# Kernel optimization log

Hardware: AMD Instinct MI355X
Metric: run time of the kernel (lower is better)

## Reference

```python
import jax, jax.numpy as jnp
import numpy as np

STDP_LR = 0.005
V_TH = 1.0  # IFNode default threshold, hard reset to 0


def setup_inputs() -> dict:
    key = jax.random.key(0)
    k1, k2 = jax.random.split(key)
    T, B, D, H = 50, 256, 1024, 2048
    x_seq = jax.random.uniform(k1, (T, B, D), dtype=jnp.float32)
    # Linear(D, H, bias=False) default init: U(-1/sqrt(D), 1/sqrt(D)), weight shape [H, D]
    bound = 1.0 / np.sqrt(D)
    weight = jax.random.uniform(k2, (H, D), dtype=jnp.float32, minval=-bound, maxval=bound)
    return {"x_seq": x_seq, "weight": weight}


def _spike(v_minus_th):
    # forward: Heaviside (surrogate only matters for backward)
    return (v_minus_th >= 0).astype(v_minus_th.dtype)


def reference(x_seq, weight):
    T, B, D = x_seq.shape
    H = weight.shape[0]
    inv_b = jnp.float32(1.0 / B)

    def step(carry, x):
        w, v = carry  # w: [H, D], v: [B, H] membrane potential (persists across t)
        mem = x @ w.T                      # [B, H]
        v = v + mem                        # IF integrate
        s = _spike(v - V_TH)               # [B, H] spikes
        v = v * (1.0 - s)                  # hard reset to 0 where spiked
        # dw.mean(0).T == lr * (1/B) * x^T s, shape [H, D] after transpose -> 'bi,bh->hi'
        dw = STDP_LR * inv_b * jnp.einsum('bi,bh->hi', x, s)
        w = w + dw                         # in-place .data update in torch
        return (w, v), s

    v0 = jnp.zeros((B, H), dtype=x_seq.dtype)
    (_, _), s_all = jax.lax.scan(step, (weight, v0), x_seq)
    spike_trace = s_all.sum(axis=0)        # [B, H]
    return spike_trace
```

## Files before the change

### kernel.cpp

```cpp
#include <hip/hip_runtime.h>
#include <hip/hip_bf16.h>


#define T_STEPS 50
#define BATCH   256
#define DIM     1024
#define HID     2048
#define HT      16
#define LR_OVER_B (0.005f / 256.0f)

#define SMEM_BYTES (65536 + 32768 + 32768 + 4096)

typedef __attribute__((ext_vector_type(8))) short short8v;
typedef __attribute__((ext_vector_type(4))) float f32x4;
typedef __attribute__((ext_vector_type(4))) int   i32x4;

static __device__ __forceinline__ ushort f32_to_bf16u(float f) {
    __hip_bfloat16 h = __float2bfloat16(f);
    return __builtin_bit_cast(unsigned short, h);
}
static __device__ __forceinline__ float bf16u_to_f32(ushort u) {
    __hip_bfloat16 h = __builtin_bit_cast(__hip_bfloat16, u);
    return __bfloat162float(h);
}

#define MFMA_B16 __builtin_amdgcn_mfma_f32_16x16x32_bf16
#define MFMA_I8  __builtin_amdgcn_mfma_i32_16x16x64_i8

__global__ __launch_bounds__(256) void prep_fwd(
    const float* __restrict__ x, ushort* __restrict__ XF)
{
    __shared__ float xs[16 * 1024];
    const int t  = blockIdx.x >> 4;
    const int bt = blockIdx.x & 15;
    const float* xrow = x + ((size_t)t * BATCH + bt * 16) * DIM;
    for (int i = threadIdx.x; i < 16 * 1024 / 4; i += 256)
        ((float4*)xs)[i] = ((const float4*)xrow)[i];
    __syncthreads();

    ushort* outb = XF + ((size_t)t * 16 + bt) * (32 * 2 * 512);
    for (int item = threadIdx.x; item < 32 * 64; item += 256) {
        const int c = item >> 6;
        const int l = item & 63;
        const int row = l & 15;
        const int col = c * 32 + (l >> 4) * 8;
        short8v hv, lv;
#pragma unroll
        for (int j = 0; j < 8; ++j) {
            float v = xs[row * 1024 + col + j];
            ushort h = f32_to_bf16u(v);
            hv[j] = (short)h;
            lv[j] = (short)f32_to_bf16u(v - bf16u_to_f32(h));
        }
        *(short8v*)(outb + ((size_t)c * 2 + 0) * 512 + l * 8) = hv;
        *(short8v*)(outb + ((size_t)c * 2 + 1) * 512 + l * 8) = lv;
    }
}

__global__ __launch_bounds__(256) void prep_xq(
    const float* __restrict__ x, unsigned char* __restrict__ XQ)
{
    __shared__ ushort q14[256 * 16];
    const int t  = blockIdx.x >> 6;
    const int dt = blockIdx.x & 63;
    {
        const int b = threadIdx.x;
        const float* src = x + ((size_t)t * BATCH + b) * DIM + dt * 16;
#pragma unroll
        for (int k = 0; k < 16; ++k) {
            int u = (int)(src[k] * 16384.0f + 0.5f);
            q14[b * 16 + k] = (ushort)(u > 16383 ? 16383 : u);
        }
    }
    __syncthreads();

    unsigned char* outb = XQ + ((size_t)t * 64 + dt) * 8192;
    const int c = threadIdx.x >> 6;
    const int l = threadIdx.x & 63;
    unsigned char hi16[16], lo16[16];
#pragma unroll
    for (int jj = 0; jj < 16; ++jj) {
        const int b2 = c * 64 + (l >> 4) * 16 + jj;
        ushort v = q14[b2 * 16 + (l & 15)];
        hi16[jj] = (unsigned char)(v >> 7);
        lo16[jj] = (unsigned char)(v & 127);
    }
    *(i32x4*)(outb + c * 2048 + l * 16)        = *(i32x4*)hi16;
    *(i32x4*)(outb + c * 2048 + 1024 + l * 16) = *(i32x4*)lo16;
}

__global__ __launch_bounds__(1024, 1) void stdp_big(
    const ushort* __restrict__ XF, const unsigned char* __restrict__ XQ,
    const float* __restrict__ weight, float* __restrict__ out)
{
    extern __shared__ char smem[];
    float*  wfs = (float*)smem;
    ushort* whF = (ushort*)(smem + 65536);
    ushort* wlF = whF + 32 * 512;
    unsigned char* slQ = (unsigned char*)(smem + 65536 + 32768 + 32768);

    const int tid  = threadIdx.x;
    const int lane = tid & 63;
    const int w    = tid >> 6;
    const int h0   = blockIdx.x * HT;

    const int fr = lane & 15;
    const int rq = (lane >> 4) * 4;

    for (int i = tid; i < 32 * 64; i += 1024) {
        const int cc  = i >> 6;
        const int l   = i & 63;
        const int row = l & 15;
        const int col = cc * 32 + (l >> 4) * 8;
        const float* src = &weight[(size_t)(h0 + row) * DIM + col];
        short8v hv, lv;
#pragma unroll
        for (int j = 0; j < 8; ++j) {
            float v = src[j];
            ushort h = f32_to_bf16u(v);
            hv[j] = (short)h;
            lv[j] = (short)f32_to_bf16u(v - bf16u_to_f32(h));
        }
        *(short8v*)&whF[cc * 512 + l * 8] = hv;
        *(short8v*)&wlF[cc * 512 + l * 8] = lv;
    }
    for (int i = tid; i < 64 * 64; i += 1024) {
        const int dt = i >> 6;
        const int l  = i & 63;
        const int h  = l & 15;
        const int d  = dt * 16 + (l >> 4) * 4;
        *(float4*)&wfs[(size_t)i * 4] =
            *(const float4*)&weight[(size_t)(h0 + h) * DIM + d];
    }
    __syncthreads();

    const f32x4 z4 = {0.f, 0.f, 0.f, 0.f};
    const i32x4 zi = {0, 0, 0, 0};
    f32x4 vmem = z4;
    f32x4 trc  = z4;

    short8v GA[2][2], GB[2][2];
    i32x4 FH[4], FL[4];

#define LDP(F, base, p) do { _Pragma("unroll") \
    for (int c_ = 0; c_ < 2; ++c_) { \
        const int cc_ = (p) * 2 + c_; \
        F[c_][0] = *(const short8v*)((base) + ((size_t)cc_ * 2 + 0) * 512); \
        F[c_][1] = *(const short8v*)((base) + ((size_t)cc_ * 2 + 1) * 512); } } while (0)

#define MFP(F, p) do { _Pragma("unroll") \
    for (int c_ = 0; c_ < 2; ++c_) { \
        const int cc_ = (p) * 2 + c_; \
        short8v bh_ = *(const short8v*)&whF[cc_ * 512 + lane * 8]; \
        short8v bl_ = *(const short8v*)&wlF[cc_ * 512 + lane * 8]; \
        acc = MFMA_B16(F[c_][0], bh_, acc, 0, 0, 0); \
        acc = MFMA_B16(F[c_][0], bl_, acc, 0, 0, 0); \
        acc = MFMA_B16(F[c_][1], bh_, acc, 0, 0, 0); } } while (0)

    {
        const ushort* wb0 = XF + (size_t)w * (32 * 2 * 512) + lane * 8;
        LDP(GA, wb0, 0);
    }

    for (int t = 0; t < T_STEPS; ++t) {
        const ushort* wbase = XF + (size_t)t * (16 * 32 * 2 * 512)
                            + (size_t)w * (32 * 2 * 512) + lane * 8;

        f32x4 acc = z4;
#pragma unroll 1
        for (int it = 0; it < 7; ++it) {
            LDP(GB, wbase, 2 * it + 1);
            MFP(GA, 2 * it);
            LDP(GA, wbase, 2 * it + 2);
            MFP(GB, 2 * it + 1);
        }
        LDP(GB, wbase, 15);
        MFP(GA, 14);
        MFP(GB, 15);

        {
            unsigned sword = 0;
#pragma unroll
            for (int j = 0; j < 4; ++j) {
                float nv = vmem[j] + acc[j];
                bool fire = (nv >= 1.0f);
                vmem[j] = fire ? 0.0f : nv;
                trc[j] += fire ? 1.0f : 0.0f;
                sword |= (fire ? 1u : 0u) << (8 * j);
            }
            *(unsigned*)&slQ[(w >> 2) * 1024 + ((w & 3) * 16 + fr) * 16 + rq] = sword;
        }

        if (t >= T_STEPS - 1) break;

        const unsigned char* xqt = XQ + (size_t)t * (64 * 8192);
        {
            const unsigned char* tb = xqt + (size_t)(w * 4) * 8192 + lane * 16;
#pragma unroll
            for (int c = 0; c < 4; ++c) {
                FH[c] = *(const i32x4*)(tb + c * 2048);
                FL[c] = *(const i32x4*)(tb + c * 2048 + 1024);
            }
        }

        __syncthreads();

#pragma unroll
        for (int q = 0; q < 4; ++q) {
            const int dt = w * 4 + q;
            i32x4 aH = zi, aL = zi;
#pragma unroll
            for (int c = 0; c < 4; ++c) {
                i32x4 sf = *(const i32x4*)&slQ[c * 1024 + lane * 16];
                aH = MFMA_I8(FH[c], sf, aH, 0, 0, 0);
                aL = MFMA_I8(FL[c], sf, aL, 0, 0, 0);
            }
            if (q < 3) {
                const unsigned char* tb = xqt + (size_t)(dt + 1) * 8192 + lane * 16;
#pragma unroll
                for (int c = 0; c < 4; ++c) {
                    FH[c] = *(const i32x4*)(tb + c * 2048);
                    FL[c] = *(const i32x4*)(tb + c * 2048 + 1024);
                }
            }
            {
                float4* wp = (float4*)&wfs[((size_t)dt * 64 + lane) * 4];
                float4 wv = *wp;
                float* wvp = &wv.x;
                ushort4 hi4, lo4;
                ushort* hp = &hi4.x; ushort* lp = &lo4.x;
#pragma unroll
                for (int j = 0; j < 4; ++j) {
                    float du = (float)(aH[j] * 128 + aL[j]) * (1.0f / 16384.0f);
                    float nw = fmaf(LR_OVER_B, du, wvp[j]);
                    wvp[j] = nw;
                    ushort hb = f32_to_bf16u(nw);
                    hp[j] = hb;
                    lp[j] = f32_to_bf16u(nw - bf16u_to_f32(hb));
                }
                *wp = wv;
                const int l_w = fr | (((dt & 1) * 2 + (rq >> 3)) << 4);
                const int off = (dt >> 1) * 512 + l_w * 8 + (rq & 4);
                *(ushort4*)&whF[off] = hi4;
                *(ushort4*)&wlF[off] = lo4;
            }
            __builtin_amdgcn_sched_barrier(0);
        }

        {
            const ushort* wbn = XF + (size_t)(t + 1) * (16 * 32 * 2 * 512)
                              + (size_t)w * (32 * 2 * 512) + lane * 8;
            LDP(GA, wbn, 0);
        }

        __syncthreads();
    }
#undef LDP
#undef MFP

#pragma unroll
    for (int j = 0; j < 4; ++j) {
        const int b = w * 16 + rq + j;
        out[(size_t)b * HID + h0 + fr] = trc[j];
    }
}

#define BK 16
__global__ __launch_bounds__(256) void stdp_fwd_if(
    const float* __restrict__ x, const float* __restrict__ w,
    float* __restrict__ v, float* __restrict__ s, float* __restrict__ trace)
{
    __shared__ float as[BK][64];
    __shared__ float bs[BK][64];
    const int tid = threadIdx.x;
    const int tx = tid & 15, ty = tid >> 4;
    const int b0 = blockIdx.y * 64, h0 = blockIdx.x * 64;
    const int row = tid >> 2, kq = (tid & 3) * 4;
    float acc[4][4] = {};
    for (int k0 = 0; k0 < DIM; k0 += BK) {
        float4 ga = *(const float4*)&x[(size_t)(b0 + row) * DIM + k0 + kq];
        float4 gb = *(const float4*)&w[(size_t)(h0 + row) * DIM + k0 + kq];
        __syncthreads();
        as[kq + 0][row] = ga.x; as[kq + 1][row] = ga.y;
        as[kq + 2][row] = ga.z; as[kq + 3][row] = ga.w;
        bs[kq + 0][row] = gb.x; bs[kq + 1][row] = gb.y;
        bs[kq + 2][row] = gb.z; bs[kq + 3][row] = gb.w;
        __syncthreads();
#pragma unroll
        for (int kk = 0; kk < BK; ++kk) {
            float4 af = *(const float4*)&as[kk][ty * 4];
            float4 bf = *(const float4*)&bs[kk][tx * 4];
            float av[4] = {af.x, af.y, af.z, af.w};
            float bv[4] = {bf.x, bf.y, bf.z, bf.w};
#pragma unroll
            for (int m = 0; m < 4; ++m)
#pragma unroll
                for (int n = 0; n < 4; ++n)
                    acc[m][n] = fmaf(av[m], bv[n], acc[m][n]);
        }
    }
#pragma unroll
    for (int m = 0; m < 4; ++m) {
        size_t idx = (size_t)(b0 + ty * 4 + m) * HID + h0 + tx * 4;
        float4 vv = *(float4*)&v[idx];
        float4 tr = *(float4*)&trace[idx];
        float4 sv;
        float* vvp = &vv.x; float* trp = &tr.x; float* svp = &sv.x;
#pragma unroll
        for (int n = 0; n < 4; ++n) {
            float nv = vvp[n] + acc[m][n];
            float sp = (nv >= 1.0f) ? 1.0f : 0.0f;
            vvp[n] = (nv >= 1.0f) ? 0.0f : nv;
            svp[n] = sp; trp[n] += sp;
        }
        *(float4*)&v[idx] = vv;
        *(float4*)&s[idx] = sv;
        *(float4*)&trace[idx] = tr;
    }
}

__global__ __launch_bounds__(256) void stdp_wupd(
    const float* __restrict__ x, const float* __restrict__ s,
    float* __restrict__ w)
{
    __shared__ float ss[BK][64];
    __shared__ float xs[BK][64];
    const int tid = threadIdx.x;
    const int tx = tid & 15, ty = tid >> 4;
    const int h0 = blockIdx.y * 64, d0 = blockIdx.x * 64;
    const int krow = tid >> 4, c4 = (tid & 15) * 4;
    float acc[4][4] = {};
    for (int bk0 = 0; bk0 < BATCH; bk0 += BK) {
        float4 gs = *(const float4*)&s[(size_t)(bk0 + krow) * HID + h0 + c4];
        float4 gx = *(const float4*)&x[(size_t)(bk0 + krow) * DIM + d0 + c4];
        __syncthreads();
        *(float4*)&ss[krow][c4] = gs;
        *(float4*)&xs[krow][c4] = gx;
        __syncthreads();
#pragma unroll
        for (int kk = 0; kk < BK; ++kk) {
            float4 af = *(const float4*)&ss[kk][ty * 4];
            float4 bf = *(const float4*)&xs[kk][tx * 4];
            float av[4] = {af.x, af.y, af.z, af.w};
            float bv[4] = {bf.x, bf.y, bf.z, bf.w};
#pragma unroll
            for (int m = 0; m < 4; ++m)
#pragma unroll
                for (int n = 0; n < 4; ++n)
                    acc[m][n] = fmaf(av[m], bv[n], acc[m][n]);
        }
    }
#pragma unroll
    for (int m = 0; m < 4; ++m) {
        size_t idx = (size_t)(h0 + ty * 4 + m) * DIM + d0 + tx * 4;
        float4 wv = *(float4*)&w[idx];
        wv.x = fmaf(LR_OVER_B, acc[m][0], wv.x);
        wv.y = fmaf(LR_OVER_B, acc[m][1], wv.y);
        wv.z = fmaf(LR_OVER_B, acc[m][2], wv.z);
        wv.w = fmaf(LR_OVER_B, acc[m][3], wv.w);
        *(float4*)&w[idx] = wv;
    }
}

extern "C" void kernel_launch(void* const* d_in, const int* in_sizes, int n_in,
                              void* d_out, int out_size, void* d_ws, size_t ws_size,
                              hipStream_t stream) {
    (void)in_sizes; (void)n_in;
    const float* x_seq  = (const float*)d_in[0];
    const float* weight = (const float*)d_in[1];
    float* out = (float*)d_out;

    const size_t WN = (size_t)HID * DIM;
    const size_t BH = (size_t)BATCH * HID;
    const size_t XN = (size_t)T_STEPS * BATCH * DIM;

    const size_t need = 6 * XN;

    if (ws_size >= need) {
        ushort* XF = (ushort*)d_ws;
        unsigned char* XQ = (unsigned char*)(XF + 2 * XN);

        prep_fwd<<<T_STEPS * 16, 256, 0, stream>>>(x_seq, XF);
        prep_xq<<<T_STEPS * 64, 256, 0, stream>>>(x_seq, XQ);

        hipFuncSetAttribute(reinterpret_cast<const void*>(&stdp_big),
                            hipFuncAttributeMaxDynamicSharedMemorySize,
                            SMEM_BYTES);
        stdp_big<<<HID / HT, 1024, SMEM_BYTES, stream>>>(
            XF, XQ, weight, out);
    } else {
        float* w = (float*)d_ws;
        float* v = w + WN;
        float* s = v + BH;
        hipMemcpyAsync(w, weight, WN * 4, hipMemcpyDeviceToDevice, stream);
        hipMemsetAsync(v, 0, BH * 4, stream);
        hipMemsetAsync(out, 0, (size_t)out_size * 4, stream);
        dim3 blkA(256), grdA(HID / 64, BATCH / 64);
        dim3 blkB(256), grdB(DIM / 64, HID / 64);
        for (int t = 0; t < T_STEPS; ++t) {
            const float* xt = x_seq + (size_t)t * BATCH * DIM;
            stdp_fwd_if<<<grdA, blkA, 0, stream>>>(xt, w, v, s, out);
            if (t < T_STEPS - 1) {
                stdp_wupd<<<grdB, blkB, 0, stream>>>(xt, s, w);
            }
        }
    }
}
```

Before: 705.7 us.

## Split each hidden slab across two blocks exchanging spikes via global flags

```diff
diff --git a/kernel.cpp b/kernel.cpp
--- a/kernel.cpp
+++ b/kernel.cpp
@@ -9,7 +9,7 @@
 #define HT      16
 #define LR_OVER_B (0.005f / 256.0f)
 
-#define SMEM_BYTES (65536 + 32768 + 32768 + 4096)
+#define SMEM_BYTES (65536 + 32768 + 32768 + 4096 + 8192)
 
 typedef __attribute__((ext_vector_type(8))) short short8v;
 typedef __attribute__((ext_vector_type(4))) float f32x4;
@@ -89,23 +89,37 @@
     *(i32x4*)(outb + c * 2048 + 1024 + l * 16) = *(i32x4*)lo16;
 }
 
-__global__ __launch_bounds__(1024, 1) void stdp_big(
+__global__ __launch_bounds__(1024, 1) void stdp_pair2(
     const ushort* __restrict__ XF, const unsigned char* __restrict__ XQ,
-    const float* __restrict__ weight, float* __restrict__ out)
+    const float* __restrict__ weight, float* __restrict__ out,
+    unsigned char* __restrict__ sex,
+    unsigned* __restrict__ flagS)
 {
     extern __shared__ char smem[];
     float*  wfs = (float*)smem;
     ushort* whF = (ushort*)(smem + 65536);
     ushort* wlF = whF + 32 * 512;
-    unsigned char* slQ = (unsigned char*)(smem + 65536 + 32768 + 32768);
-
+    unsigned char* slQ = (unsigned char*)(smem + 131072);
+    float* red = (float*)(smem + 135168);
+
+    const int bid  = blockIdx.x;
+    const int slab = bid & 127;
+    const int half = bid >> 7;
     const int tid  = threadIdx.x;
     const int lane = tid & 63;
     const int w    = tid >> 6;
-    const int h0   = blockIdx.x * HT;
+    const int h0   = slab * HT;
 
     const int fr = lane & 15;
     const int rq = (lane >> 4) * 4;
+
+    const int btl   = w & 7;
+    const int kbase = (w >> 3) * 16;
+
+    unsigned char* sex_s = sex + (size_t)bid * 2048;
+    const unsigned char* sex_p = sex + (size_t)(bid ^ 128) * 2048;
+    unsigned* flag_s = &flagS[bid];
+    unsigned* flag_p = &flagS[bid ^ 128];
 
     for (int i = tid; i < 32 * 64; i += 1024) {
         const int cc  = i >> 6;
@@ -144,13 +158,13 @@
 
 #define LDP(F, base, p) do { _Pragma("unroll") \
     for (int c_ = 0; c_ < 2; ++c_) { \
-        const int cc_ = (p) * 2 + c_; \
+        const int cc_ = kbase + (p) * 2 + c_; \
         F[c_][0] = *(const short8v*)((base) + ((size_t)cc_ * 2 + 0) * 512); \
         F[c_][1] = *(const short8v*)((base) + ((size_t)cc_ * 2 + 1) * 512); } } while (0)
 
 #define MFP(F, p) do { _Pragma("unroll") \
     for (int c_ = 0; c_ < 2; ++c_) { \
-        const int cc_ = (p) * 2 + c_; \
+        const int cc_ = kbase + (p) * 2 + c_; \
         short8v bh_ = *(const short8v*)&whF[cc_ * 512 + lane * 8]; \
         short8v bl_ = *(const short8v*)&wlF[cc_ * 512 + lane * 8]; \
         acc = MFMA_B16(F[c_][0], bh_, acc, 0, 0, 0); \
@@ -158,27 +172,44 @@
         acc = MFMA_B16(F[c_][1], bh_, acc, 0, 0, 0); } } while (0)
 
     {
-        const ushort* wb0 = XF + (size_t)w * (32 * 2 * 512) + lane * 8;
+        const ushort* wb0 = XF + (size_t)(half * 8 + btl) * (32 * 2 * 512) + lane * 8;
         LDP(GA, wb0, 0);
     }
 
     for (int t = 0; t < T_STEPS; ++t) {
         const ushort* wbase = XF + (size_t)t * (16 * 32 * 2 * 512)
-                            + (size_t)w * (32 * 2 * 512) + lane * 8;
+                            + (size_t)(half * 8 + btl) * (32 * 2 * 512) + lane * 8;
 
         f32x4 acc = z4;
 #pragma unroll 1
-        for (int it = 0; it < 7; ++it) {
+        for (int it = 0; it < 3; ++it) {
             LDP(GB, wbase, 2 * it + 1);
             MFP(GA, 2 * it);
             LDP(GA, wbase, 2 * it + 2);
             MFP(GB, 2 * it + 1);
         }
-        LDP(GB, wbase, 15);
-        MFP(GA, 14);
-        MFP(GB, 15);
-
+        LDP(GB, wbase, 7);
+        MFP(GA, 6);
+        MFP(GB, 7);
+
+        if (w >= 8)
+            *(f32x4*)&red[((w & 7) * 64 + lane) * 4] = acc;
+
+        const unsigned char* xqt = XQ + (size_t)t * (64 * 8192);
         {
+            const unsigned char* tb = xqt + (size_t)(w * 4) * 8192 + lane * 16;
+#pragma unroll
+            for (int c = 0; c < 4; ++c) {
+                FH[c] = *(const i32x4*)(tb + c * 2048);
+                FL[c] = *(const i32x4*)(tb + c * 2048 + 1024);
+            }
+        }
+
+        __syncthreads();
+
+        if (w < 8) {
+            f32x4 r = *(const f32x4*)&red[(w * 64 + lane) * 4];
+            acc = acc + r;
             unsigned sword = 0;
 #pragma unroll
             for (int j = 0; j < 4; ++j) {
@@ -188,21 +219,31 @@
                 trc[j] += fire ? 1.0f : 0.0f;
                 sword |= (fire ? 1u : 0u) << (8 * j);
             }
-            *(unsigned*)&slQ[(w >> 2) * 1024 + ((w & 3) * 16 + fr) * 16 + rq] = sword;
+            const int soff = (w >> 2) * 1024 + ((w & 3) * 16 + fr) * 16 + rq;
+            *(unsigned*)&slQ[half * 2048 + soff] = sword;
+            if (t < T_STEPS - 1) {
+                *(unsigned*)&sex_s[soff] = sword;
+                __threadfence();
+            }
         }
 
         if (t >= T_STEPS - 1) break;
 
-        const unsigned char* xqt = XQ + (size_t)t * (64 * 8192);
-        {
-            const unsigned char* tb = xqt + (size_t)(w * 4) * 8192 + lane * 16;
-#pragma unroll
-            for (int c = 0; c < 4; ++c) {
-                FH[c] = *(const i32x4*)(tb + c * 2048);
-                FL[c] = *(const i32x4*)(tb + c * 2048 + 1024);
-            }
-        }
-
+        __syncthreads();
+
+        if (tid == 0) {
+            __hip_atomic_store(flag_s, (unsigned)(t + 1),
+                               __ATOMIC_RELEASE, __HIP_MEMORY_SCOPE_AGENT);
+            while (__hip_atomic_load(flag_p, __ATOMIC_ACQUIRE,
+                                     __HIP_MEMORY_SCOPE_AGENT) < (unsigned)(t + 1))
+                __builtin_amdgcn_s_sleep(1);
+        }
+        __syncthreads();
+
+        if (tid < 128) {
+            i32x4 v = *(const i32x4*)(sex_p + tid * 16);
+            *(i32x4*)&slQ[(1 - half) * 2048 + tid * 16] = v;
+        }
         __syncthreads();
 
 #pragma unroll
@@ -249,7 +290,7 @@
 
         {
             const ushort* wbn = XF + (size_t)(t + 1) * (16 * 32 * 2 * 512)
-                              + (size_t)w * (32 * 2 * 512) + lane * 8;
+                              + (size_t)(half * 8 + btl) * (32 * 2 * 512) + lane * 8;
             LDP(GA, wbn, 0);
         }
 
@@ -258,10 +299,12 @@
 #undef LDP
 #undef MFP
 
-#pragma unroll
-    for (int j = 0; j < 4; ++j) {
-        const int b = w * 16 + rq + j;
-        out[(size_t)b * HID + h0 + fr] = trc[j];
+    if (w < 8) {
+#pragma unroll
+        for (int j = 0; j < 4; ++j) {
+            const int b = half * 128 + w * 16 + rq + j;
+            out[(size_t)b * HID + h0 + fr] = trc[j];
+        }
     }
 }
 
@@ -374,20 +417,23 @@
     const size_t BH = (size_t)BATCH * HID;
     const size_t XN = (size_t)T_STEPS * BATCH * DIM;
 
-    const size_t need = 6 * XN;
+    const size_t need = 6 * XN + 256 * 2048 + 256 * 4;
 
     if (ws_size >= need) {
         ushort* XF = (ushort*)d_ws;
         unsigned char* XQ = (unsigned char*)(XF + 2 * XN);
-
+        unsigned char* sexp = XQ + 2 * XN;
+        unsigned* flagS = (unsigned*)(sexp + 256 * 2048);
+
+        hipMemsetAsync(flagS, 0, 256 * 4, stream);
         prep_fwd<<<T_STEPS * 16, 256, 0, stream>>>(x_seq, XF);
         prep_xq<<<T_STEPS * 64, 256, 0, stream>>>(x_seq, XQ);
 
-        hipFuncSetAttribute(reinterpret_cast<const void*>(&stdp_big),
+        hipFuncSetAttribute(reinterpret_cast<const void*>(&stdp_pair2),
                             hipFuncAttributeMaxDynamicSharedMemorySize,
                             SMEM_BYTES);
-        stdp_big<<<HID / HT, 1024, SMEM_BYTES, stream>>>(
-            XF, XQ, weight, out);
+        stdp_pair2<<<256, 1024, SMEM_BYTES, stream>>>(
+            XF, XQ, weight, out, sexp, flagS);
     } else {
         float* w = (float*)d_ws;
         float* v = w + WN;
```

After: 2.417 ms. +242.6%, slower.
